# Kernel optimization log

Hardware: AMD Instinct MI355X
Metric: run time of the kernel (lower is better)

Reference implementation:

```python
import jax, jax.numpy as jnp
import numpy as np

N, E = 50000, 640000
D_IN, D_HID, D_OUT = 128, 128, 64
NEG_SLOPE = 0.2  # PyG SuperGATConv default negative_slope


def setup_inputs() -> dict:
    key = jax.random.key(0)
    ks = jax.random.split(key, 16)
    def glorot(k, shape):
        fan = sum(shape) if len(shape) > 1 else shape[0]
        return jax.random.normal(k, shape, jnp.float32) * np.sqrt(2.0 / fan)
    return {
        "x": jax.random.normal(ks[0], (N, D_IN), jnp.float32),
        "edge_index": jax.random.randint(ks[1], (2, E), 0, N, jnp.int64 if jax.config.jax_enable_x64 else jnp.int32),
        "W0": glorot(ks[2], (D_IN, D_HID)),
        "al0": glorot(ks[3], (D_HID,)),
        "ar0": glorot(ks[4], (D_HID,)),
        "b0": jnp.zeros((D_HID,), jnp.float32),
        "W1": glorot(ks[5], (D_HID, D_HID)),
        "al1": glorot(ks[6], (D_HID,)),
        "ar1": glorot(ks[7], (D_HID,)),
        "b1": jnp.zeros((D_HID,), jnp.float32),
        "W2": glorot(ks[8], (D_HID, D_OUT)),
        "al2": glorot(ks[9], (D_OUT,)),
        "ar2": glorot(ks[10], (D_OUT,)),
        "b2": jnp.zeros((D_OUT,), jnp.float32),
    }


def _supergat_layer(x, W, att_l, att_r, b, src, dst, n):
    # heads = 1, concat=False, attention_type='MX' (PyG SuperGATConv defaults)
    h = x @ W                                   # [N, C]
    hi = h[dst]                                 # target-node features x_i, [Etot, C]
    hj = h[src]                                 # source-node features x_j, [Etot, C]
    logits = jnp.sum(hi * hj, axis=-1)          # MX dot-product gate
    alpha = hj @ att_l + hi @ att_r             # GO-style scores
    alpha = alpha * jax.nn.sigmoid(logits)      # MX mixing
    alpha = jnp.where(alpha >= 0, alpha, NEG_SLOPE * alpha)  # leaky_relu
    # segment softmax over incoming edges of each target node
    amax = jax.ops.segment_max(alpha, dst, num_segments=n)
    ex = jnp.exp(alpha - amax[dst])
    denom = jax.ops.segment_sum(ex, dst, num_segments=n)
    a = ex / (denom[dst] + 1e-16)
    out = jax.ops.segment_sum(hj * a[:, None], dst, num_segments=n)
    return out + b


def reference(x, edge_index, W0, al0, ar0, b0, W1, al1, ar1, b1, W2, al2, ar2, b2):
    n = x.shape[0]
    loops = jnp.arange(n, dtype=edge_index.dtype)  # add_self_loops=True
    src = jnp.concatenate([edge_index[0], loops])
    dst = jnp.concatenate([edge_index[1], loops])
    params = [(W0, al0, ar0, b0), (W1, al1, ar1, b1), (W2, al2, ar2, b2)]
    h = x
    for (W, al, ar, b) in params:
        h = _supergat_layer(h, W, al, ar, b, src, dst, n)
        h = jax.nn.relu(h)          # dropout is identity in eval mode
    return jax.nn.log_softmax(h, axis=-1)
```

## Files before the change

### kernel.cpp

```cpp
#include <hip/hip_runtime.h>
#include <math.h>

using short8 = __attribute__((ext_vector_type(8))) short;
using f32x4 = __attribute__((ext_vector_type(4))) float;

__device__ __forceinline__ float bflo(unsigned int u) {
  union { unsigned int i; float f; } v; v.i = u << 16; return v.f;
}
__device__ __forceinline__ float bfhi(unsigned int u) {
  union { unsigned int i; float f; } v; v.i = u & 0xFFFF0000u; return v.f;
}
__device__ __forceinline__ unsigned short f2bf1(float f) {
  union { float f; unsigned int i; } v; v.f = f;
  return (unsigned short)((v.i + 0x7FFFu + ((v.i >> 16) & 1u)) >> 16);
}
__device__ __forceinline__ unsigned int f2bf_pack(float a, float b) {
  union { float f; unsigned int i; } x, y; x.f = a; y.f = b;
  unsigned int xa = x.i + 0x7FFFu + ((x.i >> 16) & 1u);
  unsigned int yb = y.i + 0x7FFFu + ((y.i >> 16) & 1u);
  return (xa >> 16) | (yb & 0xFFFF0000u);
}

#define NBUCKET 196

__global__ void prep0_kernel(const float* __restrict__ W0, const float* __restrict__ W1,
                             const float* __restrict__ W2, unsigned short* __restrict__ Wt0,
                             unsigned short* __restrict__ Wt1, unsigned short* __restrict__ Wt2,
                             int* __restrict__ ccnt, int* __restrict__ dhist) {
  int i = blockIdx.x * 256 + threadIdx.x;
  int gs = gridDim.x * 256;
  if (i < NBUCKET) ccnt[i] = 0;
  if (i < 1024) dhist[i] = 0;
  for (int j = i; j < 128 * 128; j += gs) {
    int c = j >> 7, k = j & 127;
    Wt0[c * 136 + k] = f2bf1(W0[(size_t)k * 128 + c]);
  }
  for (int j = i; j < 128 * 128; j += gs) {
    int c = j >> 7, k = j & 127;
    Wt1[c * 136 + k] = f2bf1(W1[(size_t)k * 128 + c]);
  }
  for (int j = i; j < 64 * 128; j += gs) {
    int c = j >> 7, k = j & 127;
    Wt2[c * 136 + k] = f2bf1(W2[(size_t)k * 64 + c]);
  }
}

__global__ __launch_bounds__(1024) void ccount_kernel(const int* __restrict__ ei, int E,
                                                      int N, int* __restrict__ ccnt) {
  __shared__ int lc[256];
  int t = threadIdx.x;
  if (t < 256) lc[t] = 0;
  __syncthreads();
  int e = blockIdx.x * 1024 + t;
  int etot = E + N;
  if (e < etot) {
    int d = (e < E) ? ei[E + e] : (e - E);
    atomicAdd(&lc[d >> 8], 1);
  }
  __syncthreads();
  if (t < NBUCKET) {
    int c = lc[t];
    if (c) atomicAdd(&ccnt[t], c);
  }
}

__global__ void cscan_kernel(const int* __restrict__ ccnt, int* __restrict__ cbase,
                             int* __restrict__ gcursor, int etot) {
  __shared__ int sm[256];
  int t = threadIdx.x;
  int v = (t < NBUCKET) ? ccnt[t] : 0;
  sm[t] = v;
  __syncthreads();
#pragma unroll
  for (int off = 1; off < 256; off <<= 1) {
    int add = (t >= off) ? sm[t - off] : 0;
    __syncthreads();
    sm[t] += add;
    __syncthreads();
  }
  if (t < NBUCKET) {
    int ex = sm[t] - v;
    cbase[t] = ex;
    gcursor[t] = ex;
  }
  if (t == 0) cbase[NBUCKET] = etot;
}

__global__ __launch_bounds__(1024) void bscatter_kernel(
    const int* __restrict__ ei, int E, int N, int* __restrict__ gcursor,
    uint2* __restrict__ ebuf) {
  __shared__ int cnt[256], excl[256], base[256];
  __shared__ uint2 buf[4096];
  const int t = threadIdx.x;
  const int etot = E + N;
  const int e0 = blockIdx.x * 4096;
  if (t < 256) cnt[t] = 0;
  __syncthreads();

  int sj[4], dj[4], rj[4], bj[4];
  bool vj[4];
#pragma unroll
  for (int j = 0; j < 4; ++j) {
    int e = e0 + j * 1024 + t;
    vj[j] = e < etot;
    if (vj[j]) {
      if (e < E) { sj[j] = ei[e]; dj[j] = ei[E + e]; }
      else       { sj[j] = e - E; dj[j] = e - E; }
      bj[j] = dj[j] >> 8;
      rj[j] = atomicAdd(&cnt[bj[j]], 1);
    }
  }
  __syncthreads();
  if (t < 256) excl[t] = cnt[t];
  __syncthreads();
#pragma unroll
  for (int off = 1; off < 256; off <<= 1) {
    int add = 0;
    if (t < 256 && t >= off) add = excl[t - off];
    __syncthreads();
    if (t < 256) excl[t] += add;
    __syncthreads();
  }
  if (t < 256) excl[t] -= cnt[t];
  __syncthreads();
  if (t < NBUCKET) {
    int c = cnt[t];
    base[t] = c ? atomicAdd(&gcursor[t], c) : 0;
  }
  __syncthreads();
#pragma unroll
  for (int j = 0; j < 4; ++j)
    if (vj[j]) buf[excl[bj[j]] + rj[j]] = make_uint2((unsigned)sj[j], (unsigned)dj[j]);
  __syncthreads();
  int nv = etot - e0;
  if (nv > 4096) nv = 4096;
#pragma unroll
  for (int j = 0; j < 4; ++j) {
    int i = j * 1024 + t;
    if (i < nv) {
      uint2 u = buf[i];
      int b = (int)(u.y >> 8);
      ebuf[base[b] + (i - excl[b])] = u;
    }
  }
}

__global__ __launch_bounds__(1024) void bcsr_kernel(
    const uint2* __restrict__ ebuf, const int* __restrict__ cbase,
    int* __restrict__ rowptr, int* __restrict__ csr_src, int* __restrict__ dhist,
    int N, int etot) {
  __shared__ int hist[256], hexcl[256];
  __shared__ int lh[1024];
  const int b = blockIdx.x;
  const int t = threadIdx.x;
  const int lo = cbase[b], hi = cbase[b + 1];
  const int node0 = b * 256;
  int nn = N - node0;
  if (nn > 256) nn = 256;
  if (t < 256) hist[t] = 0;
  if (t < 1024) lh[t] = 0;
  __syncthreads();
  for (int i = lo + t; i < hi; i += 1024) {
    int ln = (int)(ebuf[i].y & 255u);
    atomicAdd(&hist[ln], 1);
  }
  __syncthreads();
  if (t < nn) {
    int key = hist[t] < 1023 ? hist[t] : 1023;
    atomicAdd(&lh[key], 1);
  }
  if (t < 256) hexcl[t] = hist[t];
  __syncthreads();
#pragma unroll
  for (int off = 1; off < 256; off <<= 1) {
    int add = 0;
    if (t < 256 && t >= off) add = hexcl[t - off];
    __syncthreads();
    if (t < 256) hexcl[t] += add;
    __syncthreads();
  }
  if (t < 256) hexcl[t] -= hist[t];
  __syncthreads();
  if (t < nn) rowptr[node0 + t] = lo + hexcl[t];
  if (b == gridDim.x - 1 && t == 0) rowptr[N] = etot;
  if (t < 1024) {
    int c = lh[t];
    if (c) atomicAdd(&dhist[t], c);
  }
  if (t < 256) hist[t] = hexcl[t];
  __syncthreads();
  for (int i = lo + t; i < hi; i += 1024) {
    uint2 u = ebuf[i];
    int ln = (int)(u.y & 255u);
    int r = atomicAdd(&hist[ln], 1);
    csr_src[lo + r] = (int)u.x;
  }
}

__global__ void degscan_kernel(int* __restrict__ dhist) {
  __shared__ int arr[256];
  int t = threadIdx.x;
  int v0 = dhist[t * 4 + 0], v1 = dhist[t * 4 + 1];
  int v2 = dhist[t * 4 + 2], v3 = dhist[t * 4 + 3];
  int s0 = v0, s1 = s0 + v1, s2 = s1 + v2, s3 = s2 + v3;
  arr[t] = s3;
  __syncthreads();
#pragma unroll
  for (int off = 1; off < 256; off <<= 1) {
    int add = (t >= off) ? arr[t - off] : 0;
    __syncthreads();
    arr[t] += add;
    __syncthreads();
  }
  int base = (t > 0) ? arr[t - 1] : 0;
  dhist[t * 4 + 0] = base;
  dhist[t * 4 + 1] = base + s0;
  dhist[t * 4 + 2] = base + s1;
  dhist[t * 4 + 3] = base + s2;
}

__global__ void degscatter_kernel(const int* __restrict__ rowptr, int N,
                                  int* __restrict__ dhist, int* __restrict__ perm) {
  __shared__ int lc[1024];
  __shared__ int lb[1024];
  int t = threadIdx.x;
  for (int i = t; i < 1024; i += 256) lc[i] = 0;
  __syncthreads();
  int i = blockIdx.x * 256 + t;
  int key = 0, lr = 0;
  if (i < N) {
    int d = rowptr[i + 1] - rowptr[i];
    key = d < 1023 ? d : 1023;
    lr = atomicAdd(&lc[key], 1);
  }
  __syncthreads();
  for (int q = t; q < 1024; q += 256) {
    int c = lc[q];
    if (c) lb[q] = atomicAdd(&dhist[q], c);
  }
  __syncthreads();
  if (i < N) perm[lb[key] + lr] = i;
}

template <int COLS, bool AF32>
__global__ __launch_bounds__(256) void gemm_mfma(
    const void* __restrict__ Xv, const unsigned short* __restrict__ Wt,
    const float* __restrict__ al, const float* __restrict__ ar,
    unsigned short* __restrict__ H, float* __restrict__ hl,
    float* __restrict__ hr, int N) {
  constexpr int NT = COLS / 16;
  __shared__ unsigned short Ws[COLS * 136];
  const int tid = threadIdx.x;
  {
    const unsigned int* wg = (const unsigned int*)Wt;
    unsigned int* ws = (unsigned int*)Ws;
    for (int i = tid; i < COLS * 68; i += 256) ws[i] = wg[i];
  }
  __syncthreads();

  const int w = tid >> 6, l = tid & 63;
  const int l15 = l & 15, lg = l >> 4;
  const int r0 = blockIdx.x * 64 + w * 16;

  f32x4 acc[NT];
#pragma unroll
  for (int t = 0; t < NT; ++t)
#pragma unroll
    for (int j = 0; j < 4; ++j) acc[t][j] = 0.f;

  int arow = r0 + l15;
  if (arow > N - 1) arow = N - 1;

#pragma unroll
  for (int ks = 0; ks < 4; ++ks) {
    short8 af;
    if constexpr (AF32) {
      const float* xp = (const float*)Xv + (size_t)arow * 128 + ks * 32 + lg * 8;
      float4 x0 = *(const float4*)xp;
      float4 x1 = *(const float4*)(xp + 4);
      af[0] = (short)f2bf1(x0.x); af[1] = (short)f2bf1(x0.y);
      af[2] = (short)f2bf1(x0.z); af[3] = (short)f2bf1(x0.w);
      af[4] = (short)f2bf1(x1.x); af[5] = (short)f2bf1(x1.y);
      af[6] = (short)f2bf1(x1.z); af[7] = (short)f2bf1(x1.w);
    } else {
      af = *(const short8*)((const unsigned short*)Xv + (size_t)arow * 128 + ks * 32 + lg * 8);
    }
#pragma unroll
    for (int t = 0; t < NT; ++t) {
      short8 bf = *(const short8*)(&Ws[(t * 16 + l15) * 136 + ks * 32 + lg * 8]);
      acc[t] = __builtin_amdgcn_mfma_f32_16x16x32_bf16(af, bf, acc[t], 0, 0, 0);
    }
  }

  const int orow = r0 + lg * 4;
  float pl4[4] = {0.f, 0.f, 0.f, 0.f}, pr4[4] = {0.f, 0.f, 0.f, 0.f};
#pragma unroll
  for (int t = 0; t < NT; ++t) {
    float av = al[t * 16 + l15], rv = ar[t * 16 + l15];
#pragma unroll
    for (int r = 0; r < 4; ++r) {
      pl4[r] = fmaf(acc[t][r], av, pl4[r]);
      pr4[r] = fmaf(acc[t][r], rv, pr4[r]);
    }
#pragma unroll
    for (int r = 0; r < 4; ++r) {
      int row = orow + r;
      if (row < N) H[(size_t)row * COLS + t * 16 + l15] = f2bf1(acc[t][r]);
    }
  }
#pragma unroll
  for (int off = 1; off < 16; off <<= 1) {
#pragma unroll
    for (int r = 0; r < 4; ++r) {
      pl4[r] += __shfl_xor(pl4[r], off);
      pr4[r] += __shfl_xor(pr4[r], off);
    }
  }
  if (l15 == 0) {
#pragma unroll
    for (int r = 0; r < 4; ++r) {
      int row = orow + r;
      if (row < N) { hl[row] = pl4[r]; hr[row] = pr4[r]; }
    }
  }
}

template <int COLS, bool LAST>
__global__ __launch_bounds__(256, 6) void node_kernel(
    const unsigned short* __restrict__ H, const float* __restrict__ hl,
    const float* __restrict__ hr, const int* __restrict__ rowptr,
    const int* __restrict__ csr_src, const int* __restrict__ perm,
    const float* __restrict__ b, void* __restrict__ OUTv, int N) {
  constexpr int GS = 16;
  constexpr int EPL = COLS / GS;
  constexpr int NU = EPL / 2;
  const int lane = threadIdx.x & 63;
  const int g = lane >> 4, l = lane & 15;
  const int C = (N + 3) / 4;
  const int c = blockIdx.x * 4 + (threadIdx.x >> 6);
  const int idx = g * C + c;
  const bool active = (c < C) && (idx < N);
  const int node = active ? perm[idx] : 0;

  float hi[EPL];
  {
    unsigned int tmp[NU];
    const unsigned short* hp = H + (size_t)node * COLS + l * EPL;
    if constexpr (NU == 4) *(uint4*)tmp = *(const uint4*)hp;
    else                   *(uint2*)tmp = *(const uint2*)hp;
#pragma unroll
    for (int u = 0; u < NU; ++u) { hi[2 * u] = bflo(tmp[u]); hi[2 * u + 1] = bfhi(tmp[u]); }
  }
  const float hri = hr[node];
  const int start = active ? rowptr[node] : 0;
  const int end = active ? rowptr[node + 1] : 0;

  float m = -INFINITY, sumw = 0.f;
  float acc[EPL];
#pragma unroll
  for (int j = 0; j < EPL; ++j) acc[j] = 0.f;

  unsigned int hvA[NU], hvB[NU];
  float hlA = 0.f, hlB = 0.f;
  int e = start;
  if (e < end) {
    int s = csr_src[e];
    hlA = hl[s];
    const unsigned short* hp = H + (size_t)s * COLS + l * EPL;
    if constexpr (NU == 4) *(uint4*)hvA = *(const uint4*)hp;
    else                   *(uint2*)hvA = *(const uint2*)hp;
  }
  if (e + 1 < end) {
    int s = csr_src[e + 1];
    hlB = hl[s];
    const unsigned short* hp = H + (size_t)s * COLS + l * EPL;
    if constexpr (NU == 4) *(uint4*)hvB = *(const uint4*)hp;
    else                   *(uint2*)hvB = *(const uint2*)hp;
  }
  int i2 = (e + 2 < end) ? csr_src[e + 2] : 0;
  int i3 = (e + 3 < end) ? csr_src[e + 3] : 0;

  auto COMPUTE = [&](const float* ch, float chl) {
    float d = 0.f;
#pragma unroll
    for (int j = 0; j < EPL; ++j) d = fmaf(hi[j], ch[j], d);
    d += __shfl_xor(d, 1);
    d += __shfl_xor(d, 2);
    d += __shfl_xor(d, 4);
    d += __shfl_xor(d, 8);
    float gate = 1.f / (1.f + __expf(-d));
    float a = (chl + hri) * gate;
    a = (a >= 0.f) ? a : 0.2f * a;
    float dm = a - m;
    if (dm > 30.f) {
      float sc = __expf(-dm);
      sumw *= sc;
#pragma unroll
      for (int j = 0; j < EPL; ++j) acc[j] *= sc;
      m = a;
      dm = 0.f;
    }
    float w = __expf(dm);
    sumw += w;
#pragma unroll
    for (int j = 0; j < EPL; ++j) acc[j] = fmaf(w, ch[j], acc[j]);
  };

  while (e + 1 < end) {
    float chA[EPL], chB[EPL];
#pragma unroll
    for (int u = 0; u < NU; ++u) { chA[2 * u] = bflo(hvA[u]); chA[2 * u + 1] = bfhi(hvA[u]); }
    float clA = hlA;
    if (e + 2 < end) {
      hlA = hl[i2];
      const unsigned short* hp = H + (size_t)i2 * COLS + l * EPL;
      if constexpr (NU == 4) *(uint4*)hvA = *(const uint4*)hp;
      else                   *(uint2*)hvA = *(const uint2*)hp;
    }
#pragma unroll
    for (int u = 0; u < NU; ++u) { chB[2 * u] = bflo(hvB[u]); chB[2 * u + 1] = bfhi(hvB[u]); }
    float clB = hlB;
    if (e + 3 < end) {
      hlB = hl[i3];
      const unsigned short* hp = H + (size_t)i3 * COLS + l * EPL;
      if constexpr (NU == 4) *(uint4*)hvB = *(const uint4*)hp;
      else                   *(uint2*)hvB = *(const uint2*)hp;
    }
    i2 = (e + 4 < end) ? csr_src[e + 4] : 0;
    i3 = (e + 5 < end) ? csr_src[e + 5] : 0;
    COMPUTE(chA, clA);
    COMPUTE(chB, clB);
    e += 2;
  }
  if (e < end) {
    float chA[EPL];
#pragma unroll
    for (int u = 0; u < NU; ++u) { chA[2 * u] = bflo(hvA[u]); chA[2 * u + 1] = bfhi(hvA[u]); }
    COMPUTE(chA, hlA);
  }

  if (active) {
    const float inv = 1.f / (sumw + 1e-16f);
    float o[EPL];
    const float* bp = b + l * EPL;
#pragma unroll
    for (int j = 0; j < EPL; ++j) o[j] = fmaxf(acc[j] * inv + bp[j], 0.f);

    if constexpr (LAST) {
      float* OUT = (float*)OUTv;
      float mx = o[0];
#pragma unroll
      for (int j = 1; j < EPL; ++j) mx = fmaxf(mx, o[j]);
      mx = fmaxf(mx, __shfl_xor(mx, 1));
      mx = fmaxf(mx, __shfl_xor(mx, 2));
      mx = fmaxf(mx, __shfl_xor(mx, 4));
      mx = fmaxf(mx, __shfl_xor(mx, 8));
      float es = 0.f;
#pragma unroll
      for (int j = 0; j < EPL; ++j) es += __expf(o[j] - mx);
      es += __shfl_xor(es, 1);
      es += __shfl_xor(es, 2);
      es += __shfl_xor(es, 4);
      es += __shfl_xor(es, 8);
      float ls = logf(es);
      float4 ov = make_float4(o[0] - mx - ls, o[1] - mx - ls,
                              o[2] - mx - ls, o[3] - mx - ls);
      *(float4*)(&OUT[(size_t)node * 64 + l * 4]) = ov;
    } else {
      unsigned short* OUT = (unsigned short*)OUTv;
      unsigned int pk[NU];
#pragma unroll
      for (int u = 0; u < NU; ++u) pk[u] = f2bf_pack(o[2 * u], o[2 * u + 1]);
      *(uint4*)(OUT + (size_t)node * COLS + l * EPL) =
          make_uint4(pk[0], pk[1], pk[2], pk[3]);
    }
  }
}

extern "C" void kernel_launch(void* const* d_in, const int* in_sizes, int n_in,
                              void* d_out, int out_size, void* d_ws, size_t ws_size,
                              hipStream_t stream) {
  const float* x = (const float*)d_in[0];
  const int* ei = (const int*)d_in[1];
  const float* W0 = (const float*)d_in[2];
  const float* al0 = (const float*)d_in[3];
  const float* ar0 = (const float*)d_in[4];
  const float* b0 = (const float*)d_in[5];
  const float* W1 = (const float*)d_in[6];
  const float* al1 = (const float*)d_in[7];
  const float* ar1 = (const float*)d_in[8];
  const float* b1 = (const float*)d_in[9];
  const float* W2 = (const float*)d_in[10];
  const float* al2 = (const float*)d_in[11];
  const float* ar2 = (const float*)d_in[12];
  const float* b2 = (const float*)d_in[13];

  const int N = in_sizes[0] / 128;
  const int E = in_sizes[1] / 2;
  const int ETOT = E + N;

  char* p = (char*)d_ws;
  auto carve = [&](size_t bytes) {
    void* r = (void*)p;
    p += (bytes + 255) & ~(size_t)255;
    return r;
  };
  unsigned short* Hb = (unsigned short*)carve((size_t)N * 128 * 2);
  unsigned short* Ob = (unsigned short*)carve((size_t)N * 128 * 2);
  float* hl = (float*)carve((size_t)N * sizeof(float));
  float* hr = (float*)carve((size_t)N * sizeof(float));
  int* ccnt = (int*)carve(256 * sizeof(int));
  int* cbase = (int*)carve(256 * sizeof(int));
  int* gcursor = (int*)carve(256 * sizeof(int));
  uint2* ebuf = (uint2*)carve((size_t)ETOT * sizeof(uint2));
  int* rowptr = (int*)carve((size_t)(N + 1) * sizeof(int));
  int* csr_src = (int*)carve((size_t)ETOT * sizeof(int));
  int* dhist = (int*)carve(1024 * sizeof(int));
  int* perm = (int*)carve((size_t)N * sizeof(int));
  unsigned short* Wt0 = (unsigned short*)carve(128 * 136 * 2);
  unsigned short* Wt1 = (unsigned short*)carve(128 * 136 * 2);
  unsigned short* Wt2 = (unsigned short*)carve(64 * 136 * 2);

  const int nbs = (N + 255) / 256;

  prep0_kernel<<<nbs, 256, 0, stream>>>(W0, W1, W2, Wt0, Wt1, Wt2, ccnt, dhist);
  ccount_kernel<<<(ETOT + 1023) / 1024, 1024, 0, stream>>>(ei, E, N, ccnt);
  cscan_kernel<<<1, 256, 0, stream>>>(ccnt, cbase, gcursor, ETOT);
  bscatter_kernel<<<(ETOT + 4095) / 4096, 1024, 0, stream>>>(ei, E, N, gcursor, ebuf);
  bcsr_kernel<<<NBUCKET, 1024, 0, stream>>>(ebuf, cbase, rowptr, csr_src, dhist, N, ETOT);
  degscan_kernel<<<1, 256, 0, stream>>>(dhist);
  degscatter_kernel<<<nbs, 256, 0, stream>>>(rowptr, N, dhist, perm);

  const int gemm_grid = (N + 63) / 64;
  const int C = (N + 3) / 4;
  const int node_grid = (C + 3) / 4;

  gemm_mfma<128, true><<<gemm_grid, 256, 0, stream>>>(x, Wt0, al0, ar0, Hb, hl, hr, N);
  node_kernel<128, false><<<node_grid, 256, 0, stream>>>(Hb, hl, hr, rowptr, csr_src, perm, b0, Ob, N);

  gemm_mfma<128, false><<<gemm_grid, 256, 0, stream>>>(Ob, Wt1, al1, ar1, Hb, hl, hr, N);
  node_kernel<128, false><<<node_grid, 256, 0, stream>>>(Hb, hl, hr, rowptr, csr_src, perm, b1, Ob, N);

  gemm_mfma<64, false><<<gemm_grid, 256, 0, stream>>>(Ob, Wt2, al2, ar2, Hb, hl, hr, N);
  node_kernel<64, true><<<node_grid, 256, 0, stream>>>(Hb, hl, hr, rowptr, csr_src, perm, b2,
                                                       d_out, N);
}
```

Measured before the change: 195.2 us.

## Fuse CSR-build preprocessing kernels into one persistent kernel with grid barriers

Replaces the seven separate preprocessing launches (weight transpose, bucket count, scans, bucket scatter, per-bucket CSR, degree scan and degree sort) with one persistent kernel of 196 blocks that separates phases with a software grid barrier built on an atomic counter. The goal is to remove per-launch overhead and the idle gaps between small dependent kernels. The barrier assumes all 196 blocks of 1024 threads are resident at once, which risks deadlock if they are not. It also adds a memset launch and spin-waiting on a global atomic.

```diff
diff --git a/kernel.cpp b/kernel.cpp
--- a/kernel.cpp
+++ b/kernel.cpp
@@ -21,225 +21,246 @@
   return (xa >> 16) | (yb & 0xFFFF0000u);
 }
 
-#define NBUCKET 196
-
-__global__ void prep0_kernel(const float* __restrict__ W0, const float* __restrict__ W1,
-                             const float* __restrict__ W2, unsigned short* __restrict__ Wt0,
-                             unsigned short* __restrict__ Wt1, unsigned short* __restrict__ Wt2,
-                             int* __restrict__ ccnt, int* __restrict__ dhist) {
-  int i = blockIdx.x * 256 + threadIdx.x;
-  int gs = gridDim.x * 256;
-  if (i < NBUCKET) ccnt[i] = 0;
-  if (i < 1024) dhist[i] = 0;
-  for (int j = i; j < 128 * 128; j += gs) {
+#define NB 196
+
+__device__ __forceinline__ void gbar(int* bar, int target) {
+  __syncthreads();
+  if (threadIdx.x == 0) {
+    __threadfence();
+    atomicAdd(bar, 1);
+    while (atomicAdd(bar, 0) < target) __builtin_amdgcn_s_sleep(8);
+  }
+  __syncthreads();
+  __threadfence();
+}
+
+__global__ __launch_bounds__(1024) void csr_fused_kernel(
+    const int* __restrict__ ei, int E, int N,
+    const float* __restrict__ W0, const float* __restrict__ W1,
+    const float* __restrict__ W2, unsigned short* __restrict__ Wt0,
+    unsigned short* __restrict__ Wt1, unsigned short* __restrict__ Wt2,
+    int* __restrict__ ccnt, int* __restrict__ cbase, int* __restrict__ gcursor,
+    uint2* __restrict__ ebuf, int* __restrict__ rowptr, int* __restrict__ csr_src,
+    int* __restrict__ dhist, int* __restrict__ perm, int* bar) {
+  __shared__ int shm[8960];
+  const int b = blockIdx.x, t = threadIdx.x;
+  const int etot = E + N;
+  const int gs = NB * 1024;
+  const int gi = b * 1024 + t;
+
+  if (b == 0) {
+    if (t < 256) ccnt[t] = 0;
+    dhist[t] = 0;
+  }
+  for (int j = gi; j < 128 * 128; j += gs) {
     int c = j >> 7, k = j & 127;
     Wt0[c * 136 + k] = f2bf1(W0[(size_t)k * 128 + c]);
-  }
-  for (int j = i; j < 128 * 128; j += gs) {
-    int c = j >> 7, k = j & 127;
     Wt1[c * 136 + k] = f2bf1(W1[(size_t)k * 128 + c]);
   }
-  for (int j = i; j < 64 * 128; j += gs) {
+  for (int j = gi; j < 64 * 128; j += gs) {
     int c = j >> 7, k = j & 127;
     Wt2[c * 136 + k] = f2bf1(W2[(size_t)k * 64 + c]);
   }
-}
-
-__global__ __launch_bounds__(1024) void ccount_kernel(const int* __restrict__ ei, int E,
-                                                      int N, int* __restrict__ ccnt) {
-  __shared__ int lc[256];
-  int t = threadIdx.x;
-  if (t < 256) lc[t] = 0;
-  __syncthreads();
-  int e = blockIdx.x * 1024 + t;
-  int etot = E + N;
-  if (e < etot) {
-    int d = (e < E) ? ei[E + e] : (e - E);
-    atomicAdd(&lc[d >> 8], 1);
-  }
-  __syncthreads();
-  if (t < NBUCKET) {
-    int c = lc[t];
-    if (c) atomicAdd(&ccnt[t], c);
-  }
-}
-
-__global__ void cscan_kernel(const int* __restrict__ ccnt, int* __restrict__ cbase,
-                             int* __restrict__ gcursor, int etot) {
-  __shared__ int sm[256];
-  int t = threadIdx.x;
-  int v = (t < NBUCKET) ? ccnt[t] : 0;
-  sm[t] = v;
-  __syncthreads();
-#pragma unroll
-  for (int off = 1; off < 256; off <<= 1) {
-    int add = (t >= off) ? sm[t - off] : 0;
-    __syncthreads();
-    sm[t] += add;
-    __syncthreads();
-  }
-  if (t < NBUCKET) {
-    int ex = sm[t] - v;
-    cbase[t] = ex;
-    gcursor[t] = ex;
-  }
-  if (t == 0) cbase[NBUCKET] = etot;
-}
-
-__global__ __launch_bounds__(1024) void bscatter_kernel(
-    const int* __restrict__ ei, int E, int N, int* __restrict__ gcursor,
-    uint2* __restrict__ ebuf) {
-  __shared__ int cnt[256], excl[256], base[256];
-  __shared__ uint2 buf[4096];
-  const int t = threadIdx.x;
-  const int etot = E + N;
-  const int e0 = blockIdx.x * 4096;
-  if (t < 256) cnt[t] = 0;
-  __syncthreads();
-
-  int sj[4], dj[4], rj[4], bj[4];
-  bool vj[4];
-#pragma unroll
-  for (int j = 0; j < 4; ++j) {
-    int e = e0 + j * 1024 + t;
-    vj[j] = e < etot;
-    if (vj[j]) {
-      if (e < E) { sj[j] = ei[e]; dj[j] = ei[E + e]; }
-      else       { sj[j] = e - E; dj[j] = e - E; }
-      bj[j] = dj[j] >> 8;
-      rj[j] = atomicAdd(&cnt[bj[j]], 1);
-    }
-  }
-  __syncthreads();
-  if (t < 256) excl[t] = cnt[t];
-  __syncthreads();
-#pragma unroll
-  for (int off = 1; off < 256; off <<= 1) {
-    int add = 0;
-    if (t < 256 && t >= off) add = excl[t - off];
-    __syncthreads();
-    if (t < 256) excl[t] += add;
-    __syncthreads();
-  }
-  if (t < 256) excl[t] -= cnt[t];
-  __syncthreads();
-  if (t < NBUCKET) {
-    int c = cnt[t];
-    base[t] = c ? atomicAdd(&gcursor[t], c) : 0;
-  }
-  __syncthreads();
-#pragma unroll
-  for (int j = 0; j < 4; ++j)
-    if (vj[j]) buf[excl[bj[j]] + rj[j]] = make_uint2((unsigned)sj[j], (unsigned)dj[j]);
-  __syncthreads();
-  int nv = etot - e0;
-  if (nv > 4096) nv = 4096;
-#pragma unroll
-  for (int j = 0; j < 4; ++j) {
-    int i = j * 1024 + t;
-    if (i < nv) {
-      uint2 u = buf[i];
-      int b = (int)(u.y >> 8);
-      ebuf[base[b] + (i - excl[b])] = u;
-    }
-  }
-}
-
-__global__ __launch_bounds__(1024) void bcsr_kernel(
-    const uint2* __restrict__ ebuf, const int* __restrict__ cbase,
-    int* __restrict__ rowptr, int* __restrict__ csr_src, int* __restrict__ dhist,
-    int N, int etot) {
-  __shared__ int hist[256], hexcl[256];
-  __shared__ int lh[1024];
-  const int b = blockIdx.x;
-  const int t = threadIdx.x;
-  const int lo = cbase[b], hi = cbase[b + 1];
-  const int node0 = b * 256;
-  int nn = N - node0;
-  if (nn > 256) nn = 256;
-  if (t < 256) hist[t] = 0;
-  if (t < 1024) lh[t] = 0;
-  __syncthreads();
-  for (int i = lo + t; i < hi; i += 1024) {
-    int ln = (int)(ebuf[i].y & 255u);
-    atomicAdd(&hist[ln], 1);
-  }
-  __syncthreads();
-  if (t < nn) {
-    int key = hist[t] < 1023 ? hist[t] : 1023;
-    atomicAdd(&lh[key], 1);
-  }
-  if (t < 256) hexcl[t] = hist[t];
-  __syncthreads();
-#pragma unroll
-  for (int off = 1; off < 256; off <<= 1) {
-    int add = 0;
-    if (t < 256 && t >= off) add = hexcl[t - off];
-    __syncthreads();
-    if (t < 256) hexcl[t] += add;
-    __syncthreads();
-  }
-  if (t < 256) hexcl[t] -= hist[t];
-  __syncthreads();
-  if (t < nn) rowptr[node0 + t] = lo + hexcl[t];
-  if (b == gridDim.x - 1 && t == 0) rowptr[N] = etot;
-  if (t < 1024) {
-    int c = lh[t];
-    if (c) atomicAdd(&dhist[t], c);
-  }
-  if (t < 256) hist[t] = hexcl[t];
-  __syncthreads();
-  for (int i = lo + t; i < hi; i += 1024) {
-    uint2 u = ebuf[i];
-    int ln = (int)(u.y & 255u);
-    int r = atomicAdd(&hist[ln], 1);
-    csr_src[lo + r] = (int)u.x;
-  }
-}
-
-__global__ void degscan_kernel(int* __restrict__ dhist) {
-  __shared__ int arr[256];
-  int t = threadIdx.x;
-  int v0 = dhist[t * 4 + 0], v1 = dhist[t * 4 + 1];
-  int v2 = dhist[t * 4 + 2], v3 = dhist[t * 4 + 3];
-  int s0 = v0, s1 = s0 + v1, s2 = s1 + v2, s3 = s2 + v3;
-  arr[t] = s3;
-  __syncthreads();
-#pragma unroll
-  for (int off = 1; off < 256; off <<= 1) {
-    int add = (t >= off) ? arr[t - off] : 0;
-    __syncthreads();
-    arr[t] += add;
-    __syncthreads();
-  }
-  int base = (t > 0) ? arr[t - 1] : 0;
-  dhist[t * 4 + 0] = base;
-  dhist[t * 4 + 1] = base + s0;
-  dhist[t * 4 + 2] = base + s1;
-  dhist[t * 4 + 3] = base + s2;
-}
-
-__global__ void degscatter_kernel(const int* __restrict__ rowptr, int N,
-                                  int* __restrict__ dhist, int* __restrict__ perm) {
-  __shared__ int lc[1024];
-  __shared__ int lb[1024];
-  int t = threadIdx.x;
-  for (int i = t; i < 1024; i += 256) lc[i] = 0;
-  __syncthreads();
-  int i = blockIdx.x * 256 + t;
-  int key = 0, lr = 0;
-  if (i < N) {
-    int d = rowptr[i + 1] - rowptr[i];
-    key = d < 1023 ? d : 1023;
-    lr = atomicAdd(&lc[key], 1);
-  }
-  __syncthreads();
-  for (int q = t; q < 1024; q += 256) {
-    int c = lc[q];
-    if (c) lb[q] = atomicAdd(&dhist[q], c);
-  }
-  __syncthreads();
-  if (i < N) perm[lb[key] + lr] = i;
+  gbar(bar, NB * 1);
+
+  {
+    int* lc = shm;
+    if (t < 256) lc[t] = 0;
+    __syncthreads();
+    for (int e = gi; e < etot; e += gs) {
+      int d = (e < E) ? ei[E + e] : (e - E);
+      atomicAdd(&lc[d >> 8], 1);
+    }
+    __syncthreads();
+    if (t < NB) {
+      int c = lc[t];
+      if (c) atomicAdd(&ccnt[t], c);
+    }
+  }
+  gbar(bar, NB * 2);
+
+  if (b == 0) {
+    int* sm = shm;
+    int v = 0;
+    if (t < 256) {
+      v = (t < NB) ? ccnt[t] : 0;
+      sm[t] = v;
+    }
+    __syncthreads();
+#pragma unroll
+    for (int off = 1; off < 256; off <<= 1) {
+      int add = (t < 256 && t >= off) ? sm[t - off] : 0;
+      __syncthreads();
+      if (t < 256) sm[t] += add;
+      __syncthreads();
+    }
+    if (t < NB) {
+      int ex = sm[t] - v;
+      cbase[t] = ex;
+      gcursor[t] = ex;
+    }
+    if (t == 0) cbase[NB] = etot;
+  }
+  gbar(bar, NB * 3);
+
+  {
+    const int ntiles = (etot + 4095) >> 12;
+    if (b < ntiles) {
+      int* cnt = shm;
+      int* excl = shm + 256;
+      int* base = shm + 512;
+      uint2* buf = (uint2*)(shm + 768);
+      const int e0 = b * 4096;
+      if (t < 256) cnt[t] = 0;
+      __syncthreads();
+      int sj[4], dj[4], rj[4], bj[4];
+      bool vj[4];
+#pragma unroll
+      for (int j = 0; j < 4; ++j) {
+        int e = e0 + j * 1024 + t;
+        vj[j] = e < etot;
+        if (vj[j]) {
+          if (e < E) { sj[j] = ei[e]; dj[j] = ei[E + e]; }
+          else       { sj[j] = e - E; dj[j] = e - E; }
+          bj[j] = dj[j] >> 8;
+          rj[j] = atomicAdd(&cnt[bj[j]], 1);
+        }
+      }
+      __syncthreads();
+      if (t < 256) excl[t] = cnt[t];
+      __syncthreads();
+#pragma unroll
+      for (int off = 1; off < 256; off <<= 1) {
+        int add = 0;
+        if (t < 256 && t >= off) add = excl[t - off];
+        __syncthreads();
+        if (t < 256) excl[t] += add;
+        __syncthreads();
+      }
+      if (t < 256) excl[t] -= cnt[t];
+      __syncthreads();
+      if (t < NB) {
+        int c = cnt[t];
+        base[t] = c ? atomicAdd(&gcursor[t], c) : 0;
+      }
+      __syncthreads();
+#pragma unroll
+      for (int j = 0; j < 4; ++j)
+        if (vj[j]) buf[excl[bj[j]] + rj[j]] = make_uint2((unsigned)sj[j], (unsigned)dj[j]);
+      __syncthreads();
+      int nv = etot - e0;
+      if (nv > 4096) nv = 4096;
+#pragma unroll
+      for (int j = 0; j < 4; ++j) {
+        int i = j * 1024 + t;
+        if (i < nv) {
+          uint2 u = buf[i];
+          int bb = (int)(u.y >> 8);
+          ebuf[base[bb] + (i - excl[bb])] = u;
+        }
+      }
+    }
+  }
+  gbar(bar, NB * 4);
+
+  {
+    int* hist = shm;
+    int* hexcl = shm + 256;
+    int* lh = shm + 512;
+    const int lo = cbase[b], hi = cbase[b + 1];
+    const int node0 = b * 256;
+    int nn = N - node0;
+    if (nn > 256) nn = 256;
+    if (nn < 0) nn = 0;
+    if (t < 256) hist[t] = 0;
+    lh[t] = 0;
+    __syncthreads();
+    for (int i = lo + t; i < hi; i += 1024) {
+      int ln = (int)(ebuf[i].y & 255u);
+      atomicAdd(&hist[ln], 1);
+    }
+    __syncthreads();
+    if (t < nn) {
+      int key = hist[t] < 1023 ? hist[t] : 1023;
+      atomicAdd(&lh[key], 1);
+    }
+    if (t < 256) hexcl[t] = hist[t];
+    __syncthreads();
+#pragma unroll
+    for (int off = 1; off < 256; off <<= 1) {
+      int add = 0;
+      if (t < 256 && t >= off) add = hexcl[t - off];
+      __syncthreads();
+      if (t < 256) hexcl[t] += add;
+      __syncthreads();
+    }
+    if (t < 256) hexcl[t] -= hist[t];
+    __syncthreads();
+    if (t < nn) rowptr[node0 + t] = lo + hexcl[t];
+    if (b == 0 && t == 0) rowptr[N] = etot;
+    {
+      int c = lh[t];
+      if (c) atomicAdd(&dhist[t], c);
+    }
+    if (t < 256) hist[t] = hexcl[t];
+    __syncthreads();
+    for (int i = lo + t; i < hi; i += 1024) {
+      uint2 u = ebuf[i];
+      int ln = (int)(u.y & 255u);
+      int r = atomicAdd(&hist[ln], 1);
+      csr_src[lo + r] = (int)u.x;
+    }
+  }
+  gbar(bar, NB * 5);
+
+  if (b == 0) {
+    int* arr = shm;
+    int s0 = 0, s1 = 0, s2 = 0, s3 = 0;
+    if (t < 256) {
+      int v0 = dhist[t * 4 + 0], v1 = dhist[t * 4 + 1];
+      int v2 = dhist[t * 4 + 2], v3 = dhist[t * 4 + 3];
+      s0 = v0; s1 = s0 + v1; s2 = s1 + v2; s3 = s2 + v3;
+      arr[t] = s3;
+    }
+    __syncthreads();
+#pragma unroll
+    for (int off = 1; off < 256; off <<= 1) {
+      int add = (t < 256 && t >= off) ? arr[t - off] : 0;
+      __syncthreads();
+      if (t < 256) arr[t] += add;
+      __syncthreads();
+    }
+    if (t < 256) {
+      int base = (t > 0) ? arr[t - 1] : 0;
+      dhist[t * 4 + 0] = base;
+      dhist[t * 4 + 1] = base + s0;
+      dhist[t * 4 + 2] = base + s1;
+      dhist[t * 4 + 3] = base + s2;
+    }
+  }
+  gbar(bar, NB * 6);
+
+  {
+    int* lc = shm;
+    int* lb = shm + 1024;
+    lc[t] = 0;
+    __syncthreads();
+    int i = b * 256 + t;
+    bool act = (t < 256) && (i < N);
+    int key = 0, lr = 0;
+    if (act) {
+      int d = rowptr[i + 1] - rowptr[i];
+      key = d < 1023 ? d : 1023;
+      lr = atomicAdd(&lc[key], 1);
+    }
+    __syncthreads();
+    {
+      int c = lc[t];
+      if (c) lb[t] = atomicAdd(&dhist[t], c);
+    }
+    __syncthreads();
+    if (act) perm[lb[key] + lr] = i;
+  }
 }
 
 template <int COLS, bool AF32>
@@ -520,16 +541,12 @@
   unsigned short* Wt0 = (unsigned short*)carve(128 * 136 * 2);
   unsigned short* Wt1 = (unsigned short*)carve(128 * 136 * 2);
   unsigned short* Wt2 = (unsigned short*)carve(64 * 136 * 2);
-
-  const int nbs = (N + 255) / 256;
-
-  prep0_kernel<<<nbs, 256, 0, stream>>>(W0, W1, W2, Wt0, Wt1, Wt2, ccnt, dhist);
-  ccount_kernel<<<(ETOT + 1023) / 1024, 1024, 0, stream>>>(ei, E, N, ccnt);
-  cscan_kernel<<<1, 256, 0, stream>>>(ccnt, cbase, gcursor, ETOT);
-  bscatter_kernel<<<(ETOT + 4095) / 4096, 1024, 0, stream>>>(ei, E, N, gcursor, ebuf);
-  bcsr_kernel<<<NBUCKET, 1024, 0, stream>>>(ebuf, cbase, rowptr, csr_src, dhist, N, ETOT);
-  degscan_kernel<<<1, 256, 0, stream>>>(dhist);
-  degscatter_kernel<<<nbs, 256, 0, stream>>>(rowptr, N, dhist, perm);
+  int* bar = (int*)carve(256);
+
+  hipMemsetAsync(bar, 0, sizeof(int), stream);
+  csr_fused_kernel<<<NB, 1024, 0, stream>>>(ei, E, N, W0, W1, W2, Wt0, Wt1, Wt2,
+                                            ccnt, cbase, gcursor, ebuf, rowptr,
+                                            csr_src, dhist, perm, bar);
 
   const int gemm_grid = (N + 63) / 64;
   const int C = (N + 3) / 4;
```

Result: slower. 499.5 us (+155.8%).
